# Kernel optimization log

Hardware: AMD Instinct MI355X
Metric: run time of the kernel (lower is better)

The kernel has to match this reference:

```python
import jax, jax.numpy as jnp
import numpy as np

B, S, D, V = 4, 1024, 512, 8192
SCALES = [1, 2, 4, 8, 16]   # nn.Parameter init; used via int(scale.item()) -> static
WIN = 8                     # min(8, S//2) in compute_semantic_coherence
EPS = 1e-5


def layer_norm(x, g, b):
    m = x.mean(-1, keepdims=True)
    v = ((x - m) ** 2).mean(-1, keepdims=True)
    return (x - m) / jnp.sqrt(v + EPS) * g + b


def setup_inputs() -> dict:
    key = jax.random.key(0)
    ks = jax.random.split(key, 24)
    n = lambda k, shape, s=0.02: (jax.random.normal(k, shape, jnp.float32) * s)
    return {
        "embeddings": jax.random.normal(ks[0], (B, S, D), jnp.float32),
        "token_ids": jax.random.randint(ks[1], (B, S), 0, V),
        "context_mask": jnp.ones((B, S), jnp.float32),
        "token_similarity": n(ks[2], (V, V)),
        "W_scale": n(ks[3], (len(SCALES), D), 0.05), "b_scale": jnp.zeros((D,), jnp.float32),
        "W_sem": n(ks[4], (1, D), 0.05), "b_sem": jnp.zeros((D,), jnp.float32),
        "W_ctx": n(ks[5], (D, D), 0.02), "b_ctx": jnp.zeros((D,), jnp.float32),
        "W_fuse": n(ks[6], (4 * D, D), 0.02), "b_fuse": jnp.zeros((D,), jnp.float32),
        "ln1_g": jnp.ones((D,), jnp.float32), "ln1_b": jnp.zeros((D,), jnp.float32),
        "ln2_g": jnp.ones((D,), jnp.float32), "ln2_b": jnp.zeros((D,), jnp.float32),
        "ln3_g": jnp.ones((D,), jnp.float32), "ln3_b": jnp.zeros((D,), jnp.float32),
        "W_e0": n(ks[7], (D, D), 0.02), "b_e0": jnp.zeros((D,), jnp.float32),
        "W_e1": n(ks[8], (D, D), 0.02), "b_e1": jnp.zeros((D,), jnp.float32),
        "W_e2": n(ks[9], (D, D), 0.02), "b_e2": jnp.zeros((D,), jnp.float32),
    }


def _forward(embeddings, token_ids, context_mask, token_similarity,
             W_scale, b_scale, W_sem, b_sem, W_ctx, b_ctx, W_fuse, b_fuse,
             ln1_g, ln1_b, ln2_g, ln2_b, ln3_g, ln3_b,
             W_e0, b_e0, W_e1, b_e1, W_e2, b_e2):
    phases = jnp.tanh(embeddings)  # [B,S,D]

    # --- multi-scale coherence via cumulative sums + cos angle-difference identity ---
    # mean_t cos(p_t - m) = cos(m)*mean(cos p) + sin(m)*mean(sin p) over each window
    z = jnp.zeros((B, 1, D), phases.dtype)
    cum_p = jnp.concatenate([z, jnp.cumsum(phases, 1)], 1)            # [B,S+1,D]
    cum_c = jnp.concatenate([z, jnp.cumsum(jnp.cos(phases), 1)], 1)
    cum_s = jnp.concatenate([z, jnp.cumsum(jnp.sin(phases), 1)], 1)
    cols = []
    for s in SCALES:
        wm = (cum_p[:, s:] - cum_p[:, :-s]) / s   # window mean  [B,S-s+1,D]
        ac = (cum_c[:, s:] - cum_c[:, :-s]) / s   # window mean cos
        asn = (cum_s[:, s:] - cum_s[:, :-s]) / s  # window mean sin
        coh = jnp.mean(jnp.cos(wm) * ac + jnp.sin(wm) * asn, -1)      # [B,S-s+1]
        cols.append(jnp.pad(coh, ((0, 0), (0, s - 1))))               # torch leaves tail zeros
    msc = jnp.stack(cols, -1)                                         # [B,S,num_scales]
    scale_coh = msc @ W_scale + b_scale                               # [B,S,D]

    # --- semantic coherence (windowed, sim-weighted; torch takes mean over WHOLE tensor incl. batch) ---
    te = token_similarity[token_ids]                                  # [B,S,V]
    ten = te / jnp.maximum(jnp.linalg.norm(te, axis=-1, keepdims=True), 1e-12)
    tsim = jnp.einsum('biv,bjv->bij', ten, ten)                       # [B,S,S]
    off = jnp.arange(-WIN, WIN + 1)
    pos = jnp.arange(S)[:, None] + off[None, :]                       # [S,17]
    valid = (pos >= 0) & (pos < S)
    posc = jnp.clip(pos, 0, S - 1)
    pwin = phases[:, posc]                                            # [B,S,17,D]
    swin = jnp.take_along_axis(tsim, jnp.broadcast_to(posc[None], (B, S, 2 * WIN + 1)), axis=2)
    coh = jnp.cos((phases[:, :, None, :] - pwin) * swin[..., None]) * valid[None, :, :, None].astype(phases.dtype)
    counts = valid.sum(1).astype(phases.dtype)                        # [S]
    sem = coh.sum((0, 2, 3)) / (B * counts * D)                       # [S] (same scalar for all batches)
    sem = jnp.broadcast_to(sem[None, :], (B, S))[..., None]           # [B,S,1]
    sem_coh = sem @ W_sem + b_sem                                     # [B,S,D]

    # --- context coherence (context_mask path) ---
    cmean = jnp.mean(embeddings * context_mask[..., None], 1, keepdims=True)
    ctx_coh = jnp.cos(embeddings - cmean) @ W_ctx + b_ctx

    # --- local coherence ---
    lc = jnp.cos(embeddings[:, 1:] - embeddings[:, :-1])
    lc = jnp.concatenate([lc, jnp.zeros((B, 1, D), embeddings.dtype)], 1)

    allc = jnp.concatenate([scale_coh, sem_coh, ctx_coh, lc], -1)     # [B,S,4D]
    x = layer_norm(allc @ W_fuse + b_fuse, ln1_g, ln1_b)
    x = jax.nn.gelu(x, approximate=False)                             # dropout = identity (eval)
    for W, bb in ((W_e0, b_e0), (W_e1, b_e1), (W_e2, b_e2)):
        r = x
        h = layer_norm(x, ln2_g, ln2_b) @ W + bb
        x = r + jax.nn.gelu(h, approximate=False) * 0.1
    return layer_norm(x, ln3_g, ln3_b)


def reference(embeddings, token_ids, context_mask, token_similarity,
              W_scale, b_scale, W_sem, b_sem, W_ctx, b_ctx, W_fuse, b_fuse,
              ln1_g, ln1_b, ln2_g, ln2_b, ln3_g, ln3_b,
              W_e0, b_e0, W_e1, b_e1, W_e2, b_e2):
    return _forward(embeddings, token_ids, context_mask, token_similarity,
                    W_scale, b_scale, W_sem, b_sem, W_ctx, b_ctx, W_fuse, b_fuse,
                    ln1_g, ln1_b, ln2_g, ln2_b, ln3_g, ln3_b,
                    W_e0, b_e0, W_e1, b_e1, W_e2, b_e2)
```

## Files before the change

kernel.cpp:

```cpp
#include <hip/hip_runtime.h>


#define DEV __device__ __forceinline__
typedef unsigned short u16;
typedef __bf16 bf16x8 __attribute__((ext_vector_type(8)));
typedef float f32x4 __attribute__((ext_vector_type(4)));

static constexpr int S = 1024;
static constexpr int D = 512;
static constexpr int KCAT = 1088;

DEV u16 f2bf(float f) {
  unsigned u = __float_as_uint(f);
  return (u16)((u + 0x7fffu + ((u >> 16) & 1u)) >> 16);
}
DEV float gelu(float x) { return 0.5f * x * (1.f + erff(x * 0.70710678118654752f)); }
DEV float wred(float v) {
#pragma unroll
  for (int off = 32; off; off >>= 1) v += __shfl_down(v, off, 64);
  return v;
}
DEV void bred2(float& a, float& b, float* sm, int tid) {
  a = wred(a); b = wred(b);
  int w = tid >> 6;
  if ((tid & 63) == 0) { sm[w] = a; sm[w + 4] = b; }
  __syncthreads();
  a = sm[0] + sm[1] + sm[2] + sm[3];
  b = sm[4] + sm[5] + sm[6] + sm[7];
  __syncthreads();
}
DEV float qred(float v) {
  v += __shfl_xor(v, 1, 64);
  v += __shfl_xor(v, 2, 64);
  return v;
}

__global__ __launch_bounds__(256) void k_pre(const float* __restrict__ emb,
                                             const float* __restrict__ mask,
                                             float* __restrict__ ph,
                                             float* __restrict__ cmacc) {
  int blk = blockIdx.x, tid = threadIdx.x;
  if (blk < 1024) {
    int idx = blk * 256 + tid;
#pragma unroll
    for (int r = 0; r < 2; ++r, idx += 262144) {
      float4 v = ((const float4*)emb)[idx];
      float4 o;
      o.x = tanhf(v.x); o.y = tanhf(v.y); o.z = tanhf(v.z); o.w = tanhf(v.w);
      ((float4*)ph)[idx] = o;
    }
  } else {
    int r = blk - 1024, b = r >> 3, chunk = r & 7;
    float a0 = 0.f, a1 = 0.f;
    for (int s = chunk * 128; s < chunk * 128 + 128; ++s) {
      float m = mask[b * S + s];
      const float* row = emb + (size_t)(b * S + s) * D;
      a0 += row[tid] * m; a1 += row[tid + 256] * m;
    }
    atomicAdd(cmacc + b * D + tid, a0);
    atomicAdd(cmacc + b * D + tid + 256, a1);
  }
}

static constexpr int CP = 132;
__global__ __launch_bounds__(256) void k_dots(const float* __restrict__ sim,
                                              const int* __restrict__ tok,
                                              float* __restrict__ dots_raw,
                                              float* __restrict__ normsq) {
  __shared__ __align__(16) float sT[72 * CP];
  __shared__ int stok[72];
  int bx = blockIdx.x, cy = blockIdx.y, tid = threadIdx.x;
  int b = bx >> 4, g0 = (bx & 15) * 64, gidx = b * S + g0;
  if (tid < 72) {
    int p = g0 + tid;
    stok[tid] = (p < S) ? tok[b * S + p] : -1;
  }
  __syncthreads();
  const float4* sim4 = (const float4*)sim;
#pragma unroll
  for (int it = 0; it < 9; ++it) {
    int u = it * 256 + tid, r = u >> 5, q = u & 31;
    int tk = stok[r];
    float4 v = make_float4(0.f, 0.f, 0.f, 0.f);
    if (tk >= 0) v = sim4[(size_t)tk * 2048 + cy * 32 + q];
    *(float4*)&sT[r * CP + 4 * q] = v;
  }
  __syncthreads();
  int wave = tid >> 6, lane = tid & 63;
  f32x4 acc[9] = {};
  const float* base = &sT[lane * CP + wave * 32];
#pragma unroll 2
  for (int c4 = 0; c4 < 8; ++c4) {
    f32x4 va = *(const f32x4*)(base + 4 * c4);
    acc[8] += va * va;
#pragma unroll
    for (int o = 1; o <= 8; ++o) {
      f32x4 vb = *(const f32x4*)(base + o * CP + 4 * c4);
      acc[o - 1] += va * vb;
    }
  }
  __syncthreads();
  float* red = sT;
#pragma unroll
  for (int s = 0; s < 9; ++s) {
    f32x4 a = acc[s];
    red[(wave * 9 + s) * 64 + lane] = a[0] + a[1] + a[2] + a[3];
  }
  __syncthreads();
  for (int u = tid; u < 576; u += 256) {
    int s = u >> 6, a = u & 63;
    float v = red[s * 64 + a] + red[(9 + s) * 64 + a] +
              red[(18 + s) * 64 + a] + red[(27 + s) * 64 + a];
    if (s < 8) atomicAdd(&dots_raw[(size_t)(gidx + a) * 8 + s], v);
    else       atomicAdd(&normsq[gidx + a], v);
  }
}

static constexpr int CP2 = 68;
__global__ __launch_bounds__(256) void k_coh(const float* __restrict__ ph,
                                             const float* __restrict__ dots_raw,
                                             const float* __restrict__ normsq,
                                             float* __restrict__ msc_raw,
                                             float* __restrict__ semacc) {
  __shared__ __align__(16) float sP[88 * CP2];
  __shared__ float sw2[64 * 17];
  int bx = blockIdx.x, dy = blockIdx.y, tid = threadIdx.x;
  int b = bx >> 4, g0 = (bx & 15) * 64;
  const float4* ph4 = (const float4*)ph;
#pragma unroll
  for (int it = 0; it < 6; ++it) {
    int u = it * 256 + tid;
    if (u < 1408) {
      int r = u >> 4, q = u & 15;
      int gr = g0 - 8 + r;
      gr = gr < 0 ? 0 : (gr > S - 1 ? S - 1 : gr);
      float4 v = ph4[(size_t)(b * S + gr) * 128 + dy * 16 + q];
      *(float4*)&sP[r * CP2 + 4 * q] = v;
    }
  }
  for (int u = tid; u < 1088; u += 256) {
    int a = u / 17, oi = u - a * 17;
    int i = g0 + a, o = oi - 8, j = i + o;
    int idx = b * S + i;
    float v = 0.f;
    if (j >= 0 && j < S) {
      if (o == 0) v = 1.f;
      else {
        float dr = (o > 0) ? dots_raw[(size_t)idx * 8 + o - 1]
                           : dots_raw[(size_t)(idx + o) * 8 + (-o - 1)];
        float ni = fmaxf(sqrtf(normsq[idx]), 1e-12f);
        float nj = fmaxf(sqrtf(normsq[idx + o]), 1e-12f);
        v = dr / (ni * nj);
      }
    }
    sw2[u] = v;
  }
  __syncthreads();
  int ar = tid >> 2, dq = tid & 3;
  int i = g0 + ar, idx = b * S + i;
  int jmax = S - 1 - i; if (jmax > 15) jmax = 15;
  float swr[17];
#pragma unroll
  for (int oi = 0; oi < 17; ++oi) swr[oi] = sw2[ar * 17 + oi];
  float a0 = 0.f, a1 = 0.f, a2 = 0.f, a3 = 0.f, a4 = 0.f, asem = 0.f;
#pragma unroll 2
  for (int dd = 0; dd < 16; ++dd) {
    int d = dq + 4 * dd;
    const float* pb = &sP[(ar + 8) * CP2 + d];
    float sp = 0.f, sc = 0.f, ss = 0.f;
#pragma unroll
    for (int j = 0; j < 16; ++j) {
      float x = (j <= jmax) ? pb[j * CP2] : 0.f;
      sp += x; sc += __cosf(x); ss += __sinf(x);
      if (j == 0) a0 += __cosf(sp) * sc + __sinf(sp) * ss;
      else if (j == 1)  { float wm = sp * 0.5f;    a1 += __cosf(wm) * (sc * 0.5f)    + __sinf(wm) * (ss * 0.5f); }
      else if (j == 3)  { float wm = sp * 0.25f;   a2 += __cosf(wm) * (sc * 0.25f)   + __sinf(wm) * (ss * 0.25f); }
      else if (j == 7)  { float wm = sp * 0.125f;  a3 += __cosf(wm) * (sc * 0.125f)  + __sinf(wm) * (ss * 0.125f); }
      else if (j == 15) { float wm = sp * 0.0625f; a4 += __cosf(wm) * (sc * 0.0625f) + __sinf(wm) * (ss * 0.0625f); }
    }
    float p0 = pb[0];
    const float* qb = &sP[ar * CP2 + d];
#pragma unroll
    for (int oi = 0; oi < 17; ++oi) {
      int j = i + oi - 8;
      bool valid = (j >= 0) && (j < S);
      float pj = qb[oi * CP2];
      asem += valid ? __cosf((p0 - pj) * swr[oi]) : 0.f;
    }
  }
  a0 = qred(a0); a1 = qred(a1); a2 = qred(a2); a3 = qred(a3); a4 = qred(a4);
  asem = qred(asem);
  if (dq == 0) {
    float* mr = msc_raw + (size_t)idx * 5;
    atomicAdd(mr + 0, a0); atomicAdd(mr + 1, a1); atomicAdd(mr + 2, a2);
    atomicAdd(mr + 3, a3); atomicAdd(mr + 4, a4);
    atomicAdd(semacc + i, asem);
  }
}

__global__ __launch_bounds__(256) void k_wbig(const float* __restrict__ W0,
    const float* __restrict__ W1, const float* __restrict__ W2,
    const float* __restrict__ Wf, const float* __restrict__ wctx,
    const float* __restrict__ Wsc, const float* __restrict__ Wsm,
    const float* __restrict__ bsc, const float* __restrict__ bsm,
    const float* __restrict__ bcx,
    u16* __restrict__ T0, u16* __restrict__ T1, u16* __restrict__ T2,
    u16* __restrict__ wcatT, float* __restrict__ ctx_acc,
    float* __restrict__ sm_acc) {
  __shared__ float tile[64][65];
  int blk = blockIdx.x, tid = threadIdx.x;
  if (blk < 256) {
    int z = blk >> 6, rem = blk & 63;
    const float* src = z == 0 ? W0 : z == 1 ? W1 : z == 2 ? W2 : Wf + (size_t)1536 * 512;
    int r0 = (rem >> 3) * 64, c0 = (rem & 7) * 64;
    int tr = tid >> 6, tc = tid & 63;
#pragma unroll 4
    for (int i = 0; i < 16; ++i)
      tile[tr + i * 4][tc] = src[(size_t)(r0 + tr + i * 4) * 512 + c0 + tc];
    __syncthreads();
#pragma unroll 4
    for (int i = 0; i < 16; ++i) {
      int n = c0 + tr + i * 4, k = r0 + tc;
      u16 v = f2bf(tile[tc][tr + i * 4]);
      if (z == 3) wcatT[(size_t)n * KCAT + 512 + k] = v;
      else (z == 0 ? T0 : z == 1 ? T1 : T2)[(size_t)n * 512 + k] = v;
    }
  } else if (blk < 512) {
    int rem = blk - 256;
    int n = (rem & 1) * 256 + tid;
    int kbase = ((rem & 63) >> 1) * 16;
    int j0 = (rem >> 6) * 128;
    float acc[16] = {};
    for (int j = j0; j < j0 + 128; ++j) {
      float wf3 = Wf[(size_t)(1024 + j) * 512 + n];
#pragma unroll
      for (int kk = 0; kk < 16; ++kk) acc[kk] += wctx[(size_t)(kbase + kk) * 512 + j] * wf3;
    }
#pragma unroll
    for (int kk = 0; kk < 16; ++kk)
      atomicAdd(&ctx_acc[(size_t)(kbase + kk) * 512 + n], acc[kk]);
  } else {
    int rem = blk - 512;
    int n = (rem & 1) * 256 + tid;
    int j0 = (rem >> 1) * 16;
    float a0 = 0.f, a1 = 0.f, a2 = 0.f, a3 = 0.f, a4 = 0.f, au = 0.f, ac = 0.f;
    for (int j = j0; j < j0 + 16; ++j) {
      float wf1 = Wf[(size_t)j * 512 + n];
      float wf2 = Wf[(size_t)(512 + j) * 512 + n];
      float wf3 = Wf[(size_t)(1024 + j) * 512 + n];
      a0 += Wsc[j] * wf1; a1 += Wsc[512 + j] * wf1; a2 += Wsc[1024 + j] * wf1;
      a3 += Wsc[1536 + j] * wf1; a4 += Wsc[2048 + j] * wf1;
      au += Wsm[j] * wf2;
      ac += bsc[j] * wf1 + bsm[j] * wf2 + bcx[j] * wf3;
    }
    atomicAdd(&sm_acc[0 * 512 + n], a0);
    atomicAdd(&sm_acc[1 * 512 + n], a1);
    atomicAdd(&sm_acc[2 * 512 + n], a2);
    atomicAdd(&sm_acc[3 * 512 + n], a3);
    atomicAdd(&sm_acc[4 * 512 + n], a4);
    atomicAdd(&sm_acc[5 * 512 + n], au);
    atomicAdd(&sm_acc[6 * 512 + n], ac);
  }
}

__global__ __launch_bounds__(256) void k_packfin(const float* __restrict__ ctx_acc,
    const float* __restrict__ sm_acc, const float* __restrict__ bfu,
    u16* __restrict__ wcatT) {
  __shared__ float tile[64][65];
  int blk = blockIdx.x, tid = threadIdx.x;
  if (blk < 64) {
    int r0 = (blk >> 3) * 64, c0 = (blk & 7) * 64;
    int tr = tid >> 6, tc = tid & 63;
#pragma unroll 4
    for (int i = 0; i < 16; ++i)
      tile[tr + i * 4][tc] = ctx_acc[(size_t)(r0 + tr + i * 4) * 512 + c0 + tc];
    __syncthreads();
#pragma unroll 4
    for (int i = 0; i < 16; ++i)
      wcatT[(size_t)(c0 + tr + i * 4) * KCAT + r0 + tc] = f2bf(tile[tc][tr + i * 4]);
  } else {
    int n = (blk - 64) * 256 + tid;
    u16* row = wcatT + (size_t)n * KCAT;
#pragma unroll
    for (int s = 0; s < 6; ++s) row[1024 + s] = f2bf(sm_acc[s * 512 + n]);
    row[1030] = f2bf(sm_acc[6 * 512 + n] + bfu[n]);
    for (int k = 1031; k < KCAT; ++k) row[k] = 0;
  }
}

__global__ __launch_bounds__(256) void k_xcat(const float* __restrict__ emb,
    const float* __restrict__ cmacc, const float* __restrict__ msc_raw,
    const float* __restrict__ semacc, u16* __restrict__ xcat) {
  int idx = blockIdx.x, b = idx >> 10, i = idx & 1023, tid = threadIdx.x;
  const float* erow = emb + (size_t)idx * D;
  u16* orow = xcat + (size_t)idx * KCAT;
  for (int c = tid; c < KCAT; c += 256) {
    float v;
    if (c < 512) {
      v = __cosf(erow[c] - cmacc[b * D + c] * (1.f / 1024.f));
    } else if (c < 1024) {
      int d = c - 512;
      v = (i < S - 1) ? __cosf(erow[D + d] - erow[d]) : 0.f;
    } else if (c < 1029) {
      int s = c - 1024, req = (1 << s) - 1;
      v = (S - 1 - i >= req) ? msc_raw[(size_t)idx * 5 + s] * (1.f / 512.f) : 0.f;
    } else if (c == 1029) {
      int cnt = ((i < 8) ? i : 8) + ((S - 1 - i < 8) ? (S - 1 - i) : 8) + 1;
      v = semacc[i] / (4.f * (float)cnt * 512.f);
    } else if (c == 1030) {
      v = 1.f;
    } else v = 0.f;
    orow[c] = f2bf(v);
  }
}

__global__ __launch_bounds__(256) void k_gemm(const u16* __restrict__ A,
    const u16* __restrict__ BT, float* __restrict__ C,
    const float* __restrict__ bias, int K) {
  __shared__ __align__(16) u16 sA[64 * 72];
  __shared__ __align__(16) u16 sB[64 * 72];
  int tid = threadIdx.x, wave = tid >> 6, lane = tid & 63;
  int m0 = blockIdx.x * 64, n0 = blockIdx.y * 64;
  int lr = tid >> 2, lc = (tid & 3) * 8;
  int q8 = (lane >> 4) * 8, l15 = lane & 15;
  const u16* Ap = A + (size_t)(m0 + lr) * K + lc;
  const u16* Bp = BT + (size_t)(n0 + lr) * K + lc;
  f32x4 acc[4] = {};
  for (int k0 = 0; k0 < K; k0 += 64) {
    *(uint4*)&sA[lr * 72 + lc]      = *(const uint4*)(Ap + k0);
    *(uint4*)&sA[lr * 72 + lc + 32] = *(const uint4*)(Ap + k0 + 32);
    *(uint4*)&sB[lr * 72 + lc]      = *(const uint4*)(Bp + k0);
    *(uint4*)&sB[lr * 72 + lc + 32] = *(const uint4*)(Bp + k0 + 32);
    __syncthreads();
    int row = wave * 16 + l15;
    bf16x8 af0 = *(const bf16x8*)&sA[row * 72 + q8];
    bf16x8 af1 = *(const bf16x8*)&sA[row * 72 + 32 + q8];
#pragma unroll
    for (int f = 0; f < 4; ++f) {
      bf16x8 b0 = *(const bf16x8*)&sB[(f * 16 + l15) * 72 + q8];
      bf16x8 b1 = *(const bf16x8*)&sB[(f * 16 + l15) * 72 + 32 + q8];
      acc[f] = __builtin_amdgcn_mfma_f32_16x16x32_bf16(af0, b0, acc[f], 0, 0, 0);
      acc[f] = __builtin_amdgcn_mfma_f32_16x16x32_bf16(af1, b1, acc[f], 0, 0, 0);
    }
    __syncthreads();
  }
  int r0 = m0 + wave * 16 + (lane >> 4) * 4;
#pragma unroll
  for (int f = 0; f < 4; ++f) {
    int col = n0 + f * 16 + l15;
    float bv = bias ? bias[col] : 0.f;
#pragma unroll
    for (int r = 0; r < 4; ++r)
      C[(size_t)(r0 + r) * 512 + col] = acc[f][r] + bv;
  }
}

__global__ __launch_bounds__(256) void k_post_y1(const float* __restrict__ y,
    float* __restrict__ x, u16* __restrict__ t,
    const float* __restrict__ g1, const float* __restrict__ b1,
    const float* __restrict__ g2, const float* __restrict__ b2) {
  __shared__ float sm[8];
  int row = blockIdx.x, tid = threadIdx.x;
  size_t base = (size_t)row * 512;
  float v0 = y[base + tid], v1 = y[base + tid + 256];
  float s = v0 + v1, ss = v0 * v0 + v1 * v1;
  bred2(s, ss, sm, tid);
  float m = s * (1.f / 512.f);
  float inv = rsqrtf(ss * (1.f / 512.f) - m * m + 1e-5f);
  float x0 = gelu((v0 - m) * inv * g1[tid] + b1[tid]);
  float x1 = gelu((v1 - m) * inv * g1[tid + 256] + b1[tid + 256]);
  x[base + tid] = x0; x[base + tid + 256] = x1;
  s = x0 + x1; ss = x0 * x0 + x1 * x1;
  bred2(s, ss, sm, tid);
  m = s * (1.f / 512.f);
  inv = rsqrtf(ss * (1.f / 512.f) - m * m + 1e-5f);
  t[base + tid] = f2bf((x0 - m) * inv * g2[tid] + b2[tid]);
  t[base + tid + 256] = f2bf((x1 - m) * inv * g2[tid + 256] + b2[tid + 256]);
}

__global__ __launch_bounds__(256) void k_post_res(const float* __restrict__ h,
    float* __restrict__ x, u16* __restrict__ t, float* __restrict__ out,
    const float* __restrict__ g, const float* __restrict__ bb, int final_) {
  __shared__ float sm[8];
  int row = blockIdx.x, tid = threadIdx.x;
  size_t base = (size_t)row * 512;
  float x0 = x[base + tid] + 0.1f * gelu(h[base + tid]);
  float x1 = x[base + tid + 256] + 0.1f * gelu(h[base + tid + 256]);
  float s = x0 + x1, ss = x0 * x0 + x1 * x1;
  bred2(s, ss, sm, tid);
  float m = s * (1.f / 512.f);
  float inv = rsqrtf(ss * (1.f / 512.f) - m * m + 1e-5f);
  float n0 = (x0 - m) * inv * g[tid] + bb[tid];
  float n1 = (x1 - m) * inv * g[tid + 256] + bb[tid + 256];
  if (final_) {
    out[base + tid] = n0; out[base + tid + 256] = n1;
  } else {
    x[base + tid] = x0; x[base + tid + 256] = x1;
    t[base + tid] = f2bf(n0); t[base + tid + 256] = f2bf(n1);
  }
}

extern "C" void kernel_launch(void* const* d_in, const int* in_sizes, int n_in,
                              void* d_out, int out_size, void* d_ws, size_t ws_size,
                              hipStream_t stream) {
  const float* emb     = (const float*)d_in[0];
  const int*   tok     = (const int*)d_in[1];
  const float* mask    = (const float*)d_in[2];
  const float* sim     = (const float*)d_in[3];
  const float* W_scale = (const float*)d_in[4];
  const float* b_scale = (const float*)d_in[5];
  const float* W_sem   = (const float*)d_in[6];
  const float* b_sem   = (const float*)d_in[7];
  const float* W_ctx   = (const float*)d_in[8];
  const float* b_ctx   = (const float*)d_in[9];
  const float* W_fuse  = (const float*)d_in[10];
  const float* b_fuse  = (const float*)d_in[11];
  const float* ln1_g = (const float*)d_in[12], *ln1_b = (const float*)d_in[13];
  const float* ln2_g = (const float*)d_in[14], *ln2_b = (const float*)d_in[15];
  const float* ln3_g = (const float*)d_in[16], *ln3_b = (const float*)d_in[17];
  const float* W_e0 = (const float*)d_in[18], *b_e0 = (const float*)d_in[19];
  const float* W_e1 = (const float*)d_in[20], *b_e1 = (const float*)d_in[21];
  const float* W_e2 = (const float*)d_in[22], *b_e2 = (const float*)d_in[23];
  float* out = (float*)d_out;

  char* w = (char*)d_ws; size_t off = 0;
  auto alloc = [&](size_t bytes) { void* p = w + off; off += (bytes + 255) & ~(size_t)255; return p; };
  float* phases = (float*)alloc((size_t)4096 * 512 * 4);
  float* hbuf   = (float*)alloc((size_t)4096 * 512 * 4);
  float* xbuf   = (float*)alloc((size_t)4096 * 512 * 4);
  u16*   tbuf   = (u16*)  alloc((size_t)4096 * 512 * 2);
  u16*   xcat   = (u16*)  alloc((size_t)4096 * KCAT * 2);
  u16*   wcatT  = (u16*)  alloc((size_t)512 * KCAT * 2);
  u16*   We0T   = (u16*)  alloc((size_t)512 * 512 * 2);
  u16*   We1T   = (u16*)  alloc((size_t)512 * 512 * 2);
  u16*   We2T   = (u16*)  alloc((size_t)512 * 512 * 2);
  float* semacc   = (float*)alloc((size_t)1024 * 4);
  float* cmacc    = (float*)alloc((size_t)4 * 512 * 4);
  float* dots_raw = (float*)alloc((size_t)4096 * 8 * 4);
  float* normsq   = (float*)alloc((size_t)4096 * 4);
  float* msc_raw  = (float*)alloc((size_t)4096 * 5 * 4);
  float* ctx_acc  = (float*)alloc((size_t)512 * 512 * 4);
  float* sm_acc   = (float*)alloc((size_t)7 * 512 * 4);
  (void)ws_size; (void)in_sizes; (void)n_in; (void)out_size;

  size_t zbytes = (size_t)(1024 + 4 * 512 + 4096 * 8 + 4096 + 4096 * 5 + 512 * 512 + 7 * 512) * 4;
  hipMemsetAsync(semacc, 0, zbytes, stream);

  k_pre<<<1056, 256, 0, stream>>>(emb, mask, phases, cmacc);
  k_dots<<<dim3(64, 64), 256, 0, stream>>>(sim, tok, dots_raw, normsq);
  k_coh<<<dim3(64, 8), 256, 0, stream>>>(phases, dots_raw, normsq, msc_raw, semacc);

  k_wbig<<<576, 256, 0, stream>>>(W_e0, W_e1, W_e2, W_fuse, W_ctx,
                                  W_scale, W_sem, b_scale, b_sem, b_ctx,
                                  We0T, We1T, We2T, wcatT, ctx_acc, sm_acc);
  k_packfin<<<66, 256, 0, stream>>>(ctx_acc, sm_acc, b_fuse, wcatT);

  k_xcat<<<4096, 256, 0, stream>>>(emb, cmacc, msc_raw, semacc, xcat);
  k_gemm<<<dim3(64, 8), 256, 0, stream>>>(xcat, wcatT, hbuf, nullptr, KCAT);
  k_post_y1<<<4096, 256, 0, stream>>>(hbuf, xbuf, tbuf, ln1_g, ln1_b, ln2_g, ln2_b);

  k_gemm<<<dim3(64, 8), 256, 0, stream>>>(tbuf, We0T, hbuf, b_e0, 512);
  k_post_res<<<4096, 256, 0, stream>>>(hbuf, xbuf, tbuf, nullptr, ln2_g, ln2_b, 0);
  k_gemm<<<dim3(64, 8), 256, 0, stream>>>(tbuf, We1T, hbuf, b_e1, 512);
  k_post_res<<<4096, 256, 0, stream>>>(hbuf, xbuf, tbuf, nullptr, ln2_g, ln2_b, 0);
  k_gemm<<<dim3(64, 8), 256, 0, stream>>>(tbuf, We2T, hbuf, b_e2, 512);
  k_post_res<<<4096, 256, 0, stream>>>(hbuf, xbuf, nullptr, out, ln3_g, ln3_b, 1);
}
```

Measured before the change: 591.7 us.

## Merge front-end kernels into two launches and prefetch GEMM tiles into registers

Combines the tanh/mask-sum, similarity-dot and weight-packing kernels into one k_front launch, and the coherence and final weight-pack kernels into one k_mid launch, cutting launch count and letting independent work share the GPU. The dot-product blocks now each process four column chunks, accumulating in registers, which reduces the grid and the number of atomics. The GEMM loads the next K tile into registers before the MFMA work on the current one, so global latency overlaps compute. The costs are larger heterogeneous blocks with more register pressure and less parallelism in the dots phase.

```diff
diff --git a/kernel.cpp b/kernel.cpp
--- a/kernel.cpp
+++ b/kernel.cpp
@@ -35,198 +35,120 @@
   return v;
 }
 
-__global__ __launch_bounds__(256) void k_pre(const float* __restrict__ emb,
-                                             const float* __restrict__ mask,
-                                             float* __restrict__ ph,
-                                             float* __restrict__ cmacc) {
-  int blk = blockIdx.x, tid = threadIdx.x;
-  if (blk < 1024) {
-    int idx = blk * 256 + tid;
-#pragma unroll
-    for (int r = 0; r < 2; ++r, idx += 262144) {
-      float4 v = ((const float4*)emb)[idx];
-      float4 o;
-      o.x = tanhf(v.x); o.y = tanhf(v.y); o.z = tanhf(v.z); o.w = tanhf(v.w);
-      ((float4*)ph)[idx] = o;
-    }
-  } else {
-    int r = blk - 1024, b = r >> 3, chunk = r & 7;
-    float a0 = 0.f, a1 = 0.f;
-    for (int s = chunk * 128; s < chunk * 128 + 128; ++s) {
-      float m = mask[b * S + s];
-      const float* row = emb + (size_t)(b * S + s) * D;
-      a0 += row[tid] * m; a1 += row[tid + 256] * m;
-    }
-    atomicAdd(cmacc + b * D + tid, a0);
-    atomicAdd(cmacc + b * D + tid + 256, a1);
-  }
-}
-
 static constexpr int CP = 132;
-__global__ __launch_bounds__(256) void k_dots(const float* __restrict__ sim,
-                                              const int* __restrict__ tok,
-                                              float* __restrict__ dots_raw,
-                                              float* __restrict__ normsq) {
-  __shared__ __align__(16) float sT[72 * CP];
-  __shared__ int stok[72];
-  int bx = blockIdx.x, cy = blockIdx.y, tid = threadIdx.x;
-  int b = bx >> 4, g0 = (bx & 15) * 64, gidx = b * S + g0;
-  if (tid < 72) {
-    int p = g0 + tid;
-    stok[tid] = (p < S) ? tok[b * S + p] : -1;
-  }
-  __syncthreads();
-  const float4* sim4 = (const float4*)sim;
-#pragma unroll
-  for (int it = 0; it < 9; ++it) {
-    int u = it * 256 + tid, r = u >> 5, q = u & 31;
-    int tk = stok[r];
-    float4 v = make_float4(0.f, 0.f, 0.f, 0.f);
-    if (tk >= 0) v = sim4[(size_t)tk * 2048 + cy * 32 + q];
-    *(float4*)&sT[r * CP + 4 * q] = v;
-  }
-  __syncthreads();
-  int wave = tid >> 6, lane = tid & 63;
-  f32x4 acc[9] = {};
-  const float* base = &sT[lane * CP + wave * 32];
-#pragma unroll 2
-  for (int c4 = 0; c4 < 8; ++c4) {
-    f32x4 va = *(const f32x4*)(base + 4 * c4);
-    acc[8] += va * va;
-#pragma unroll
-    for (int o = 1; o <= 8; ++o) {
-      f32x4 vb = *(const f32x4*)(base + o * CP + 4 * c4);
-      acc[o - 1] += va * vb;
-    }
-  }
-  __syncthreads();
-  float* red = sT;
-#pragma unroll
-  for (int s = 0; s < 9; ++s) {
-    f32x4 a = acc[s];
-    red[(wave * 9 + s) * 64 + lane] = a[0] + a[1] + a[2] + a[3];
-  }
-  __syncthreads();
-  for (int u = tid; u < 576; u += 256) {
-    int s = u >> 6, a = u & 63;
-    float v = red[s * 64 + a] + red[(9 + s) * 64 + a] +
-              red[(18 + s) * 64 + a] + red[(27 + s) * 64 + a];
-    if (s < 8) atomicAdd(&dots_raw[(size_t)(gidx + a) * 8 + s], v);
-    else       atomicAdd(&normsq[gidx + a], v);
-  }
-}
-
-static constexpr int CP2 = 68;
-__global__ __launch_bounds__(256) void k_coh(const float* __restrict__ ph,
-                                             const float* __restrict__ dots_raw,
-                                             const float* __restrict__ normsq,
-                                             float* __restrict__ msc_raw,
-                                             float* __restrict__ semacc) {
-  __shared__ __align__(16) float sP[88 * CP2];
-  __shared__ float sw2[64 * 17];
-  int bx = blockIdx.x, dy = blockIdx.y, tid = threadIdx.x;
-  int b = bx >> 4, g0 = (bx & 15) * 64;
-  const float4* ph4 = (const float4*)ph;
-#pragma unroll
-  for (int it = 0; it < 6; ++it) {
-    int u = it * 256 + tid;
-    if (u < 1408) {
-      int r = u >> 4, q = u & 15;
-      int gr = g0 - 8 + r;
-      gr = gr < 0 ? 0 : (gr > S - 1 ? S - 1 : gr);
-      float4 v = ph4[(size_t)(b * S + gr) * 128 + dy * 16 + q];
-      *(float4*)&sP[r * CP2 + 4 * q] = v;
-    }
-  }
-  for (int u = tid; u < 1088; u += 256) {
-    int a = u / 17, oi = u - a * 17;
-    int i = g0 + a, o = oi - 8, j = i + o;
-    int idx = b * S + i;
-    float v = 0.f;
-    if (j >= 0 && j < S) {
-      if (o == 0) v = 1.f;
-      else {
-        float dr = (o > 0) ? dots_raw[(size_t)idx * 8 + o - 1]
-                           : dots_raw[(size_t)(idx + o) * 8 + (-o - 1)];
-        float ni = fmaxf(sqrtf(normsq[idx]), 1e-12f);
-        float nj = fmaxf(sqrtf(normsq[idx + o]), 1e-12f);
-        v = dr / (ni * nj);
-      }
-    }
-    sw2[u] = v;
-  }
-  __syncthreads();
-  int ar = tid >> 2, dq = tid & 3;
-  int i = g0 + ar, idx = b * S + i;
-  int jmax = S - 1 - i; if (jmax > 15) jmax = 15;
-  float swr[17];
-#pragma unroll
-  for (int oi = 0; oi < 17; ++oi) swr[oi] = sw2[ar * 17 + oi];
-  float a0 = 0.f, a1 = 0.f, a2 = 0.f, a3 = 0.f, a4 = 0.f, asem = 0.f;
-#pragma unroll 2
-  for (int dd = 0; dd < 16; ++dd) {
-    int d = dq + 4 * dd;
-    const float* pb = &sP[(ar + 8) * CP2 + d];
-    float sp = 0.f, sc = 0.f, ss = 0.f;
-#pragma unroll
-    for (int j = 0; j < 16; ++j) {
-      float x = (j <= jmax) ? pb[j * CP2] : 0.f;
-      sp += x; sc += __cosf(x); ss += __sinf(x);
-      if (j == 0) a0 += __cosf(sp) * sc + __sinf(sp) * ss;
-      else if (j == 1)  { float wm = sp * 0.5f;    a1 += __cosf(wm) * (sc * 0.5f)    + __sinf(wm) * (ss * 0.5f); }
-      else if (j == 3)  { float wm = sp * 0.25f;   a2 += __cosf(wm) * (sc * 0.25f)   + __sinf(wm) * (ss * 0.25f); }
-      else if (j == 7)  { float wm = sp * 0.125f;  a3 += __cosf(wm) * (sc * 0.125f)  + __sinf(wm) * (ss * 0.125f); }
-      else if (j == 15) { float wm = sp * 0.0625f; a4 += __cosf(wm) * (sc * 0.0625f) + __sinf(wm) * (ss * 0.0625f); }
-    }
-    float p0 = pb[0];
-    const float* qb = &sP[ar * CP2 + d];
-#pragma unroll
-    for (int oi = 0; oi < 17; ++oi) {
-      int j = i + oi - 8;
-      bool valid = (j >= 0) && (j < S);
-      float pj = qb[oi * CP2];
-      asem += valid ? __cosf((p0 - pj) * swr[oi]) : 0.f;
-    }
-  }
-  a0 = qred(a0); a1 = qred(a1); a2 = qred(a2); a3 = qred(a3); a4 = qred(a4);
-  asem = qred(asem);
-  if (dq == 0) {
-    float* mr = msc_raw + (size_t)idx * 5;
-    atomicAdd(mr + 0, a0); atomicAdd(mr + 1, a1); atomicAdd(mr + 2, a2);
-    atomicAdd(mr + 3, a3); atomicAdd(mr + 4, a4);
-    atomicAdd(semacc + i, asem);
-  }
-}
-
-__global__ __launch_bounds__(256) void k_wbig(const float* __restrict__ W0,
-    const float* __restrict__ W1, const float* __restrict__ W2,
-    const float* __restrict__ Wf, const float* __restrict__ wctx,
-    const float* __restrict__ Wsc, const float* __restrict__ Wsm,
-    const float* __restrict__ bsc, const float* __restrict__ bsm,
-    const float* __restrict__ bcx,
+__global__ __launch_bounds__(256) void k_front(
+    const float* __restrict__ emb, const float* __restrict__ mask,
+    float* __restrict__ ph, float* __restrict__ cmacc,
+    const float* __restrict__ sim, const int* __restrict__ tok,
+    float* __restrict__ dots_raw, float* __restrict__ normsq,
+    const float* __restrict__ W0, const float* __restrict__ W1,
+    const float* __restrict__ W2, const float* __restrict__ Wf,
+    const float* __restrict__ wctx, const float* __restrict__ Wsc,
+    const float* __restrict__ Wsm, const float* __restrict__ bsc,
+    const float* __restrict__ bsm, const float* __restrict__ bcx,
     u16* __restrict__ T0, u16* __restrict__ T1, u16* __restrict__ T2,
     u16* __restrict__ wcatT, float* __restrict__ ctx_acc,
     float* __restrict__ sm_acc) {
-  __shared__ float tile[64][65];
+  __shared__ __align__(16) float smem[72 * CP];
+  __shared__ int stok[72];
   int blk = blockIdx.x, tid = threadIdx.x;
-  if (blk < 256) {
-    int z = blk >> 6, rem = blk & 63;
+
+  if (blk < 1024) {
+    int bx = blk >> 4, cyb = blk & 15;
+    int b = bx >> 4, g0 = (bx & 15) * 64, gidx = b * S + g0;
+    if (tid < 72) {
+      int p = g0 + tid;
+      stok[tid] = (p < S) ? tok[b * S + p] : -1;
+    }
+    __syncthreads();
+    const float4* sim4 = (const float4*)sim;
+    int wave = tid >> 6, lane = tid & 63;
+    f32x4 acc[9] = {};
+    for (int cc = 0; cc < 4; ++cc) {
+      int cy = cyb * 4 + cc;
+#pragma unroll
+      for (int it = 0; it < 9; ++it) {
+        int u = it * 256 + tid, r = u >> 5, q = u & 31;
+        int tk = stok[r];
+        float4 v = make_float4(0.f, 0.f, 0.f, 0.f);
+        if (tk >= 0) v = sim4[(size_t)tk * 2048 + cy * 32 + q];
+        *(float4*)&smem[r * CP + 4 * q] = v;
+      }
+      __syncthreads();
+      const float* base = &smem[lane * CP + wave * 32];
+#pragma unroll 2
+      for (int c4 = 0; c4 < 8; ++c4) {
+        f32x4 va = *(const f32x4*)(base + 4 * c4);
+        acc[8] += va * va;
+#pragma unroll
+        for (int o = 1; o <= 8; ++o) {
+          f32x4 vb = *(const f32x4*)(base + o * CP + 4 * c4);
+          acc[o - 1] += va * vb;
+        }
+      }
+      __syncthreads();
+    }
+    float* red = smem;
+#pragma unroll
+    for (int s = 0; s < 9; ++s) {
+      f32x4 a = acc[s];
+      red[(wave * 9 + s) * 64 + lane] = a[0] + a[1] + a[2] + a[3];
+    }
+    __syncthreads();
+    for (int u = tid; u < 576; u += 256) {
+      int s = u >> 6, a = u & 63;
+      float v = red[s * 64 + a] + red[(9 + s) * 64 + a] +
+                red[(18 + s) * 64 + a] + red[(27 + s) * 64 + a];
+      if (s < 8) atomicAdd(&dots_raw[(size_t)(gidx + a) * 8 + s], v);
+      else       atomicAdd(&normsq[gidx + a], v);
+    }
+    return;
+  }
+
+  if (blk < 2080) {
+    int blk2 = blk - 1024;
+    if (blk2 < 1024) {
+      int idx = blk2 * 256 + tid;
+#pragma unroll
+      for (int r = 0; r < 2; ++r, idx += 262144) {
+        float4 v = ((const float4*)emb)[idx];
+        float4 o;
+        o.x = tanhf(v.x); o.y = tanhf(v.y); o.z = tanhf(v.z); o.w = tanhf(v.w);
+        ((float4*)ph)[idx] = o;
+      }
+    } else {
+      int r = blk2 - 1024, b = r >> 3, chunk = r & 7;
+      float a0 = 0.f, a1 = 0.f;
+      for (int s = chunk * 128; s < chunk * 128 + 128; ++s) {
+        float m = mask[b * S + s];
+        const float* row = emb + (size_t)(b * S + s) * D;
+        a0 += row[tid] * m; a1 += row[tid + 256] * m;
+      }
+      atomicAdd(cmacc + b * D + tid, a0);
+      atomicAdd(cmacc + b * D + tid + 256, a1);
+    }
+    return;
+  }
+
+  int blk2 = blk - 2080;
+  if (blk2 < 256) {
+    int z = blk2 >> 6, rem = blk2 & 63;
     const float* src = z == 0 ? W0 : z == 1 ? W1 : z == 2 ? W2 : Wf + (size_t)1536 * 512;
     int r0 = (rem >> 3) * 64, c0 = (rem & 7) * 64;
     int tr = tid >> 6, tc = tid & 63;
 #pragma unroll 4
     for (int i = 0; i < 16; ++i)
-      tile[tr + i * 4][tc] = src[(size_t)(r0 + tr + i * 4) * 512 + c0 + tc];
+      smem[(tr + i * 4) * 65 + tc] = src[(size_t)(r0 + tr + i * 4) * 512 + c0 + tc];
     __syncthreads();
 #pragma unroll 4
     for (int i = 0; i < 16; ++i) {
       int n = c0 + tr + i * 4, k = r0 + tc;
-      u16 v = f2bf(tile[tc][tr + i * 4]);
+      u16 v = f2bf(smem[tc * 65 + tr + i * 4]);
       if (z == 3) wcatT[(size_t)n * KCAT + 512 + k] = v;
       else (z == 0 ? T0 : z == 1 ? T1 : T2)[(size_t)n * 512 + k] = v;
     }
-  } else if (blk < 512) {
-    int rem = blk - 256;
+  } else if (blk2 < 512) {
+    int rem = blk2 - 256;
     int n = (rem & 1) * 256 + tid;
     int kbase = ((rem & 63) >> 1) * 16;
     int j0 = (rem >> 6) * 128;
@@ -240,7 +162,7 @@
     for (int kk = 0; kk < 16; ++kk)
       atomicAdd(&ctx_acc[(size_t)(kbase + kk) * 512 + n], acc[kk]);
   } else {
-    int rem = blk - 512;
+    int rem = blk2 - 512;
     int n = (rem & 1) * 256 + tid;
     int j0 = (rem >> 1) * 16;
     float a0 = 0.f, a1 = 0.f, a2 = 0.f, a3 = 0.f, a4 = 0.f, au = 0.f, ac = 0.f;
@@ -263,23 +185,106 @@
   }
 }
 
-__global__ __launch_bounds__(256) void k_packfin(const float* __restrict__ ctx_acc,
-    const float* __restrict__ sm_acc, const float* __restrict__ bfu,
-    u16* __restrict__ wcatT) {
-  __shared__ float tile[64][65];
+static constexpr int CP2 = 68;
+__global__ __launch_bounds__(256) void k_mid(const float* __restrict__ ph,
+    const float* __restrict__ dots_raw, const float* __restrict__ normsq,
+    float* __restrict__ msc_raw, float* __restrict__ semacc,
+    const float* __restrict__ ctx_acc, const float* __restrict__ sm_acc,
+    const float* __restrict__ bfu, u16* __restrict__ wcatT) {
+  __shared__ __align__(16) float smem[7072];
   int blk = blockIdx.x, tid = threadIdx.x;
-  if (blk < 64) {
-    int r0 = (blk >> 3) * 64, c0 = (blk & 7) * 64;
+
+  if (blk < 512) {
+    float* sP = smem;
+    float* sw2 = smem + 88 * CP2;
+    int bx = blk >> 3, dy = blk & 7;
+    int b = bx >> 4, g0 = (bx & 15) * 64;
+    const float4* ph4 = (const float4*)ph;
+#pragma unroll
+    for (int it = 0; it < 6; ++it) {
+      int u = it * 256 + tid;
+      if (u < 1408) {
+        int r = u >> 4, q = u & 15;
+        int gr = g0 - 8 + r;
+        gr = gr < 0 ? 0 : (gr > S - 1 ? S - 1 : gr);
+        float4 v = ph4[(size_t)(b * S + gr) * 128 + dy * 16 + q];
+        *(float4*)&sP[r * CP2 + 4 * q] = v;
+      }
+    }
+    for (int u = tid; u < 1088; u += 256) {
+      int a = u / 17, oi = u - a * 17;
+      int i = g0 + a, o = oi - 8, j = i + o;
+      int idx = b * S + i;
+      float v = 0.f;
+      if (j >= 0 && j < S) {
+        if (o == 0) v = 1.f;
+        else {
+          float dr = (o > 0) ? dots_raw[(size_t)idx * 8 + o - 1]
+                             : dots_raw[(size_t)(idx + o) * 8 + (-o - 1)];
+          float ni = fmaxf(sqrtf(normsq[idx]), 1e-12f);
+          float nj = fmaxf(sqrtf(normsq[idx + o]), 1e-12f);
+          v = dr / (ni * nj);
+        }
+      }
+      sw2[u] = v;
+    }
+    __syncthreads();
+    int ar = tid >> 2, dq = tid & 3;
+    int i = g0 + ar, idx = b * S + i;
+    int jmax = S - 1 - i; if (jmax > 15) jmax = 15;
+    float swr[17];
+#pragma unroll
+    for (int oi = 0; oi < 17; ++oi) swr[oi] = sw2[ar * 17 + oi];
+    float a0 = 0.f, a1 = 0.f, a2 = 0.f, a3 = 0.f, a4 = 0.f, asem = 0.f;
+#pragma unroll 2
+    for (int dd = 0; dd < 16; ++dd) {
+      int d = dq + 4 * dd;
+      const float* pb = &sP[(ar + 8) * CP2 + d];
+      float sp = 0.f, sc = 0.f, ss = 0.f;
+#pragma unroll
+      for (int j = 0; j < 16; ++j) {
+        float x = (j <= jmax) ? pb[j * CP2] : 0.f;
+        sp += x; sc += __cosf(x); ss += __sinf(x);
+        if (j == 0) a0 += __cosf(sp) * sc + __sinf(sp) * ss;
+        else if (j == 1)  { float wm = sp * 0.5f;    a1 += __cosf(wm) * (sc * 0.5f)    + __sinf(wm) * (ss * 0.5f); }
+        else if (j == 3)  { float wm = sp * 0.25f;   a2 += __cosf(wm) * (sc * 0.25f)   + __sinf(wm) * (ss * 0.25f); }
+        else if (j == 7)  { float wm = sp * 0.125f;  a3 += __cosf(wm) * (sc * 0.125f)  + __sinf(wm) * (ss * 0.125f); }
+        else if (j == 15) { float wm = sp * 0.0625f; a4 += __cosf(wm) * (sc * 0.0625f) + __sinf(wm) * (ss * 0.0625f); }
+      }
+      float p0 = pb[0];
+      const float* qb = &sP[ar * CP2 + d];
+#pragma unroll
+      for (int oi = 0; oi < 17; ++oi) {
+        int j = i + oi - 8;
+        bool valid = (j >= 0) && (j < S);
+        float pj = qb[oi * CP2];
+        asem += valid ? __cosf((p0 - pj) * swr[oi]) : 0.f;
+      }
+    }
+    a0 = qred(a0); a1 = qred(a1); a2 = qred(a2); a3 = qred(a3); a4 = qred(a4);
+    asem = qred(asem);
+    if (dq == 0) {
+      float* mr = msc_raw + (size_t)idx * 5;
+      atomicAdd(mr + 0, a0); atomicAdd(mr + 1, a1); atomicAdd(mr + 2, a2);
+      atomicAdd(mr + 3, a3); atomicAdd(mr + 4, a4);
+      atomicAdd(semacc + i, asem);
+    }
+    return;
+  }
+
+  int blk2 = blk - 512;
+  if (blk2 < 64) {
+    int r0 = (blk2 >> 3) * 64, c0 = (blk2 & 7) * 64;
     int tr = tid >> 6, tc = tid & 63;
 #pragma unroll 4
     for (int i = 0; i < 16; ++i)
-      tile[tr + i * 4][tc] = ctx_acc[(size_t)(r0 + tr + i * 4) * 512 + c0 + tc];
+      smem[(tr + i * 4) * 65 + tc] = ctx_acc[(size_t)(r0 + tr + i * 4) * 512 + c0 + tc];
     __syncthreads();
 #pragma unroll 4
     for (int i = 0; i < 16; ++i)
-      wcatT[(size_t)(c0 + tr + i * 4) * KCAT + r0 + tc] = f2bf(tile[tc][tr + i * 4]);
+      wcatT[(size_t)(c0 + tr + i * 4) * KCAT + r0 + tc] = f2bf(smem[tc * 65 + tr + i * 4]);
   } else {
-    int n = (blk - 64) * 256 + tid;
+    int n = (blk2 - 64) * 256 + tid;
     u16* row = wcatT + (size_t)n * KCAT;
 #pragma unroll
     for (int s = 0; s < 6; ++s) row[1024 + s] = f2bf(sm_acc[s * 512 + n]);
@@ -325,13 +330,23 @@
   int q8 = (lane >> 4) * 8, l15 = lane & 15;
   const u16* Ap = A + (size_t)(m0 + lr) * K + lc;
   const u16* Bp = BT + (size_t)(n0 + lr) * K + lc;
+  uint4 ra0 = *(const uint4*)(Ap);
+  uint4 ra1 = *(const uint4*)(Ap + 32);
+  uint4 rb0 = *(const uint4*)(Bp);
+  uint4 rb1 = *(const uint4*)(Bp + 32);
   f32x4 acc[4] = {};
   for (int k0 = 0; k0 < K; k0 += 64) {
-    *(uint4*)&sA[lr * 72 + lc]      = *(const uint4*)(Ap + k0);
-    *(uint4*)&sA[lr * 72 + lc + 32] = *(const uint4*)(Ap + k0 + 32);
-    *(uint4*)&sB[lr * 72 + lc]      = *(const uint4*)(Bp + k0);
-    *(uint4*)&sB[lr * 72 + lc + 32] = *(const uint4*)(Bp + k0 + 32);
-    __syncthreads();
+    *(uint4*)&sA[lr * 72 + lc]      = ra0;
+    *(uint4*)&sA[lr * 72 + lc + 32] = ra1;
+    *(uint4*)&sB[lr * 72 + lc]      = rb0;
+    *(uint4*)&sB[lr * 72 + lc + 32] = rb1;
+    __syncthreads();
+    if (k0 + 64 < K) {
+      ra0 = *(const uint4*)(Ap + k0 + 64);
+      ra1 = *(const uint4*)(Ap + k0 + 96);
+      rb0 = *(const uint4*)(Bp + k0 + 64);
+      rb1 = *(const uint4*)(Bp + k0 + 96);
+    }
     int row = wave * 16 + l15;
     bf16x8 af0 = *(const bf16x8*)&sA[row * 72 + q8];
     bf16x8 af1 = *(const bf16x8*)&sA[row * 72 + 32 + q8];
@@ -446,14 +461,13 @@
   size_t zbytes = (size_t)(1024 + 4 * 512 + 4096 * 8 + 4096 + 4096 * 5 + 512 * 512 + 7 * 512) * 4;
   hipMemsetAsync(semacc, 0, zbytes, stream);
 
-  k_pre<<<1056, 256, 0, stream>>>(emb, mask, phases, cmacc);
-  k_dots<<<dim3(64, 64), 256, 0, stream>>>(sim, tok, dots_raw, normsq);
-  k_coh<<<dim3(64, 8), 256, 0, stream>>>(phases, dots_raw, normsq, msc_raw, semacc);
-
-  k_wbig<<<576, 256, 0, stream>>>(W_e0, W_e1, W_e2, W_fuse, W_ctx,
-                                  W_scale, W_sem, b_scale, b_sem, b_ctx,
-                                  We0T, We1T, We2T, wcatT, ctx_acc, sm_acc);
-  k_packfin<<<66, 256, 0, stream>>>(ctx_acc, sm_acc, b_fuse, wcatT);
+  k_front<<<2656, 256, 0, stream>>>(emb, mask, phases, cmacc,
+                                    sim, tok, dots_raw, normsq,
+                                    W_e0, W_e1, W_e2, W_fuse, W_ctx,
+                                    W_scale, W_sem, b_scale, b_sem, b_ctx,
+                                    We0T, We1T, We2T, wcatT, ctx_acc, sm_acc);
+  k_mid<<<578, 256, 0, stream>>>(phases, dots_raw, normsq, msc_raw, semacc,
+                                 ctx_acc, sm_acc, b_fuse, wcatT);
 
   k_xcat<<<4096, 256, 0, stream>>>(emb, cmacc, msc_raw, semacc, xcat);
   k_gemm<<<dim3(64, 8), 256, 0, stream>>>(xcat, wcatT, hbuf, nullptr, KCAT);
```

Result: no change. 589.8 us (-0.3%).
